# Kernel optimization log

Hardware: AMD Instinct MI355X
Metric: run time of the kernel (lower is better)

The kernel has to match this reference:

```python
import jax, jax.numpy as jnp
import numpy as np

HEADS = 8
DHEAD = 64
KSIZE = 7


def setup_inputs() -> dict:
    key = jax.random.key(0)
    k1, k2, k3, k4 = jax.random.split(key, 4)
    b, H, W, C = 16, 56, 56, 256
    inner = HEADS * DHEAD  # 512
    x = jax.random.normal(k1, (b, H, W, C), jnp.float32)
    Wq = jax.random.normal(k2, (1, 1, C, inner), jnp.float32) * 0.02
    Wkv = jax.random.normal(k3, (KSIZE, KSIZE, C, 2 * inner), jnp.float32) * 0.02
    Wo = jax.random.normal(k4, (1, 1, inner, C), jnp.float32) * 0.02
    bo = jnp.zeros((C,), jnp.float32)
    return {"x": x, "Wq": Wq, "Wkv": Wkv, "Wo": Wo, "bo": bo}


def reference(x, Wq, Wkv, Wo, bo):
    heads, dh = HEADS, DHEAD
    scale = dh ** -0.5
    b, H, W, C = x.shape
    # 1x1 conv Q projection == per-pixel matmul
    q = jnp.einsum('bhwc,cf->bhwf', x, Wq[0, 0])  # [b,H,W,inner]
    # k x k strided conv KV downsample (SAME==VALID since H%k==0)
    kv = jax.lax.conv_general_dilated(
        x, Wkv, window_strides=(KSIZE, KSIZE), padding='VALID',
        dimension_numbers=('NHWC', 'HWIO', 'NHWC'))  # [b,H/k,W/k,2*inner]
    k_, v_ = jnp.split(kv, 2, axis=-1)

    def split_heads(t):
        B, hh, ww, _ = t.shape
        return t.reshape(B, hh * ww, heads, dh)  # [b, seq, h, d]

    q = split_heads(q)      # [b, H*W, h, d]
    k_ = split_heads(k_)    # [b, (H/k)*(W/k), h, d]
    v_ = split_heads(v_)
    dots = jnp.einsum('bqhd,bkhd->bhqk', q, k_) * scale
    attn = jax.nn.softmax(dots, axis=-1)
    out = jnp.einsum('bhqk,bkhd->bqhd', attn, v_)
    out = out.reshape(b, H, W, heads * dh)
    # output 1x1 conv with bias (dropout rate 0 -> identity)
    out = jnp.einsum('bhwf,fc->bhwc', out, Wo[0, 0]) + bo
    return out
```

## Files before the change

### kernel.cpp

```cpp
#include <hip/hip_runtime.h>
#include <stdint.h>

typedef unsigned short ushort_t;
typedef __attribute__((ext_vector_type(8))) unsigned short ushort8v;
typedef __attribute__((ext_vector_type(8))) short short8v;
typedef __attribute__((ext_vector_type(4))) float f32x4;

__device__ __forceinline__ float bf2f(ushort_t u) {
  union { unsigned int i; float f; } v;
  v.i = ((unsigned int)u) << 16;
  return v.f;
}
__device__ __forceinline__ ushort_t f2bf(float f) {
  union { float f; unsigned int i; } v;
  v.f = f;
  unsigned int r = v.i + 0x7FFFu + ((v.i >> 16) & 1u);
  return (ushort_t)(r >> 16);
}

__device__ __forceinline__ ushort8v load8bf(const ushort_t* __restrict__ p) {
  return *(const ushort8v*)p;
}
__device__ __forceinline__ ushort8v load8bf(const float* __restrict__ p) {
  const float4 a = *(const float4*)p;
  const float4 b = *(const float4*)(p + 4);
  ushort8v r;
  r[0] = f2bf(a.x); r[1] = f2bf(a.y); r[2] = f2bf(a.z); r[3] = f2bf(a.w);
  r[4] = f2bf(b.x); r[5] = f2bf(b.y); r[6] = f2bf(b.z); r[7] = f2bf(b.w);
  return r;
}
__device__ __forceinline__ void storeC(float* p, float v) { *p = v; }
__device__ __forceinline__ void storeC(ushort_t* p, float v) { *p = f2bf(v); }

__device__ __forceinline__ void gl16(const ushort_t* g, ushort_t* l) {
  __builtin_amdgcn_global_load_lds(
      (const __attribute__((address_space(1))) void*)g,
      (__attribute__((address_space(3))) void*)l, 16, 0, 0);
}

__device__ __forceinline__ size_t pp_off(unsigned g) {
  const unsigned b = g / 3136u;
  const unsigned r = g - b * 3136u;
  const unsigned y = r / 56u, xx = r - y * 56u;
  const unsigned ty = y / 7u, dy = y - ty * 7u;
  const unsigned tx = xx / 7u, dx = xx - tx * 7u;
  return ((size_t)((b * 64u + ty * 8u + tx) * 49u + dy * 7u + dx)) << 8;
}

__global__ __launch_bounds__(256) void transpose_cvt(
    const float* __restrict__ W, ushort_t* __restrict__ WT, int K, int N) {
  __shared__ float tile[32][33];
  const int t = threadIdx.x;
  const int k0 = blockIdx.y * 32;
  const int n0 = blockIdx.x * 32;
  {
    const int r = t >> 3, c4 = (t & 7) * 4;
    const float4 v = *(const float4*)(W + (size_t)(k0 + r) * N + n0 + c4);
    tile[r][c4] = v.x; tile[r][c4 + 1] = v.y;
    tile[r][c4 + 2] = v.z; tile[r][c4 + 3] = v.w;
  }
  __syncthreads();
  {
    const int rn = t >> 3, ck = (t & 7) * 4;
    union { ushort_t u[4]; uint2 v; } o;
#pragma unroll
    for (int j = 0; j < 4; ++j) o.u[j] = f2bf(tile[ck + j][rn]);
    *(uint2*)(WT + (size_t)(n0 + rn) * K + k0 + ck) = o.v;
  }
}

__global__ __launch_bounds__(256) void cvt_f32_bf16(
    const float* __restrict__ in, ushort_t* __restrict__ out) {
  const int i = (blockIdx.x * 256 + threadIdx.x) * 4;
  const float4 v = *(const float4*)(in + i);
  union { ushort_t u[4]; uint2 q; } o;
  o.u[0] = f2bf(v.x); o.u[1] = f2bf(v.y);
  o.u[2] = f2bf(v.z); o.u[3] = f2bf(v.w);
  *(uint2*)(out + i) = o.q;
}

__global__ __launch_bounds__(256) void cvt_im2col(
    const float* __restrict__ x, ushort_t* __restrict__ xp) {
  const int e = (blockIdx.x * 256 + threadIdx.x) * 8;
  const unsigned p = ((unsigned)e) >> 8;
  const int c = e & 255;
  const float4 a = *(const float4*)(x + e);
  const float4 b = *(const float4*)(x + e + 4);
  ushort8v o;
  o[0] = f2bf(a.x); o[1] = f2bf(a.y); o[2] = f2bf(a.z); o[3] = f2bf(a.w);
  o[4] = f2bf(b.x); o[5] = f2bf(b.y); o[6] = f2bf(b.z); o[7] = f2bf(b.w);
  *(ushort8v*)(xp + pp_off(p) + c) = o;
}

template <int MODE, bool PERMA>
__device__ __forceinline__ void gemm_body(
    const ushort_t* __restrict__ A, const ushort_t* __restrict__ BT,
    const float* __restrict__ bias, void* __restrict__ Cv,
    int N, int K, int m0, int n0, int kbeg, int kend) {
  __shared__ ushort_t lA[2][4096];
  __shared__ ushort_t lB[2][4096];
  const int t = threadIdx.x;
  const int lane = t & 63;
  const int wv = __builtin_amdgcn_readfirstlane(t >> 6);
  const int wm = wv >> 1, wn = wv & 1;
  const int rl = lane & 15;
  const int kof = (lane >> 4) * 8;

  const ushort_t* aS[2];
  const ushort_t* bS[2];
#pragma unroll
  for (int h = 0; h < 2; ++h) {
    const int row = h * 64 + wv * 16 + rl;
    size_t aoff;
    if (PERMA)
      aoff = pp_off((unsigned)(m0 + row));
    else
      aoff = (size_t)(m0 + row) * K;
    aS[h] = A + aoff + kof;
    bS[h] = BT + (size_t)(n0 + row) * K + kof;
  }

  f32x4 acc[4][4] = {};

#pragma unroll
  for (int h = 0; h < 2; ++h) {
    gl16(aS[h] + kbeg, &lA[0][h * 2048 + wv * 512]);
    gl16(bS[h] + kbeg, &lB[0][h * 2048 + wv * 512]);
  }
  __syncthreads();

  int cur = 0;
  for (int k0 = kbeg; k0 < kend; k0 += 32) {
    const int nxt = k0 + 32;
    if (nxt < kend) {
#pragma unroll
      for (int h = 0; h < 2; ++h) {
        gl16(aS[h] + nxt, &lA[cur ^ 1][h * 2048 + wv * 512]);
        gl16(bS[h] + nxt, &lB[cur ^ 1][h * 2048 + wv * 512]);
      }
    }
    short8v af[4], bfr[4];
#pragma unroll
    for (int i = 0; i < 4; ++i) {
      af[i] = *(const short8v*)&lA[cur][(wm * 4 + i) * 512 + lane * 8];
      bfr[i] = *(const short8v*)&lB[cur][(wn * 4 + i) * 512 + lane * 8];
    }
#pragma unroll
    for (int i = 0; i < 4; ++i)
#pragma unroll
      for (int j = 0; j < 4; ++j)
        acc[i][j] = __builtin_amdgcn_mfma_f32_16x16x32_bf16(
            af[i], bfr[j], acc[i][j], 0, 0, 0);
    __syncthreads();
    cur ^= 1;
  }

  const int col = lane & 15, rq = (lane >> 4) * 4;
#pragma unroll
  for (int i = 0; i < 4; ++i) {
    const int mb = m0 + (wm * 4 + i) * 16 + rq;
#pragma unroll
    for (int j = 0; j < 4; ++j) {
      const int nb = n0 + (wn * 4 + j) * 16 + col;
      if (MODE == 0) {
        ushort_t* C = (ushort_t*)Cv;
#pragma unroll
        for (int r = 0; r < 4; ++r)
          C[(size_t)(mb + r) * N + nb] = f2bf(acc[i][j][r]);
      } else if (MODE == 1) {
        float* C = (float*)Cv;
        const float badd = bias[nb];
#pragma unroll
        for (int r = 0; r < 4; ++r)
          C[(size_t)(mb + r) * N + nb] = acc[i][j][r] + badd;
      } else {
        float* C = (float*)Cv;
#pragma unroll
        for (int r = 0; r < 4; ++r)
          atomicAdd(&C[(size_t)(mb + r) * N + nb], acc[i][j][r]);
      }
    }
  }
}

template <int MODE, bool PERMA>
__global__ __launch_bounds__(256) void gemm_nt_2d(
    const ushort_t* __restrict__ A, const ushort_t* __restrict__ BT,
    const float* __restrict__ bias, void* __restrict__ C, int N, int K) {
  gemm_body<MODE, PERMA>(A, BT, bias, C, N, K, blockIdx.y * 128,
                         blockIdx.x * 128, 0, K);
}

__global__ __launch_bounds__(256) void gemm_kv_gl(
    const ushort_t* __restrict__ xpat, const ushort_t* __restrict__ WkvT,
    float* __restrict__ C) {
  const int bl = blockIdx.x;
  const int kbeg = (bl >> 6) * 448;
  gemm_body<2, false>(xpat, WkvT, (const float*)nullptr, C, 1024, 12544,
                      (bl & 7) * 128, ((bl >> 3) & 7) * 128, kbeg, kbeg + 448);
}

template <typename TA, typename TC>
__global__ __launch_bounds__(256) void gemm_mfma_nt(
    const TA* __restrict__ A, const ushort_t* __restrict__ BT,
    const float* __restrict__ bias, TC* __restrict__ C,
    int M, int N, int K, int has_bias) {
  __shared__ ushort_t lA[8 * 512];
  __shared__ ushort_t lB[8 * 512];
  const int t = threadIdx.x;
  const int m0 = blockIdx.y * 128;
  const int n0 = blockIdx.x * 128;
  const int lane = t & 63;
  const int wm = (t >> 6) >> 1, wn = (t >> 6) & 1;

  f32x4 acc[4][4] = {};

  const int sm = t >> 2;
  const int kq = t & 3;

  for (int k0 = 0; k0 < K; k0 += 32) {
#pragma unroll
    for (int h = 0; h < 2; ++h) {
      const int m = h * 64 + sm;
      const int off = (m >> 4) * 512 + (kq * 16 + (m & 15)) * 8;
      const ushort8v av = load8bf(A + (size_t)(m0 + m) * K + k0 + kq * 8);
      *(ushort8v*)&lA[off] = av;
      const ushort8v bv = load8bf(BT + (size_t)(n0 + m) * K + k0 + kq * 8);
      *(ushort8v*)&lB[off] = bv;
    }
    __syncthreads();
    short8v af[4], bf[4];
#pragma unroll
    for (int i = 0; i < 4; ++i) {
      af[i] = *(const short8v*)&lA[(wm * 4 + i) * 512 + lane * 8];
      bf[i] = *(const short8v*)&lB[(wn * 4 + i) * 512 + lane * 8];
    }
#pragma unroll
    for (int i = 0; i < 4; ++i)
#pragma unroll
      for (int j = 0; j < 4; ++j)
        acc[i][j] = __builtin_amdgcn_mfma_f32_16x16x32_bf16(
            af[i], bf[j], acc[i][j], 0, 0, 0);
    __syncthreads();
  }

  const int col = lane & 15, rq = (lane >> 4) * 4;
#pragma unroll
  for (int i = 0; i < 4; ++i) {
    const int mb = m0 + (wm * 4 + i) * 16 + rq;
#pragma unroll
    for (int j = 0; j < 4; ++j) {
      const int nb = n0 + (wn * 4 + j) * 16 + col;
      const float badd = has_bias ? bias[nb] : 0.f;
#pragma unroll
      for (int r = 0; r < 4; ++r)
        storeC(&C[(size_t)(mb + r) * N + nb], acc[i][j][r] + badd);
    }
  }
}

template <typename TA>
__global__ __launch_bounds__(256) void gemm_kv_mfma(
    const TA* __restrict__ x, const ushort_t* __restrict__ WkvT,
    float* __restrict__ C) {
  __shared__ ushort_t lA[8 * 512];
  __shared__ ushort_t lB[8 * 512];
  const int t = threadIdx.x;
  const int bl = blockIdx.x;
  const int m0 = (bl & 7) * 128;
  const int n0 = ((bl >> 3) & 7) * 128;
  const int kbeg = (bl >> 6) * 896;
  const int lane = t & 63;
  const int wm = (t >> 6) >> 1, wn = (t >> 6) & 1;

  f32x4 acc[4][4] = {};

  const int sm = t >> 2;
  const int kq = t & 3;

  for (int k0 = kbeg; k0 < kbeg + 896; k0 += 32) {
#pragma unroll
    for (int h = 0; h < 2; ++h) {
      const int m = h * 64 + sm;
      const int off = (m >> 4) * 512 + (kq * 16 + (m & 15)) * 8;
      const int gm = m0 + m;
      const int b = gm >> 6, ty = (gm >> 3) & 7, tx = gm & 7;
      const int k = k0 + kq * 8;
      const int patch = k >> 8;
      const int c = k & 255;
      const int dy = (patch * 37) >> 8;
      const int dx = patch - dy * 7;
      const int pix = b * 3136 + (ty * 7 + dy) * 56 + (tx * 7 + dx);
      const ushort8v av = load8bf(x + (size_t)pix * 256 + c);
      *(ushort8v*)&lA[off] = av;
      const ushort8v bv =
          load8bf(WkvT + (size_t)(n0 + m) * 12544 + k0 + kq * 8);
      *(ushort8v*)&lB[off] = bv;
    }
    __syncthreads();
    short8v af[4], bf[4];
#pragma unroll
    for (int i = 0; i < 4; ++i) {
      af[i] = *(const short8v*)&lA[(wm * 4 + i) * 512 + lane * 8];
      bf[i] = *(const short8v*)&lB[(wn * 4 + i) * 512 + lane * 8];
    }
#pragma unroll
    for (int i = 0; i < 4; ++i)
#pragma unroll
      for (int j = 0; j < 4; ++j)
        acc[i][j] = __builtin_amdgcn_mfma_f32_16x16x32_bf16(
            af[i], bf[j], acc[i][j], 0, 0, 0);
    __syncthreads();
  }

  const int col = lane & 15, rq = (lane >> 4) * 4;
#pragma unroll
  for (int i = 0; i < 4; ++i) {
    const int mb = m0 + (wm * 4 + i) * 16 + rq;
#pragma unroll
    for (int j = 0; j < 4; ++j) {
      const int nb = n0 + (wn * 4 + j) * 16 + col;
#pragma unroll
      for (int r = 0; r < 4; ++r)
        atomicAdd(&C[(size_t)(mb + r) * 1024 + nb], acc[i][j][r]);
    }
  }
}

__global__ __launch_bounds__(256) void attn_mfma(
    ushort_t* __restrict__ qo, const ushort_t* __restrict__ kvb) {
  __shared__ ushort_t VT[64][72];
  __shared__ ushort_t P[4][64][72];
  const int t = threadIdx.x;
  const int lane = t & 63;
  const int w = t >> 6;
  const int bh = blockIdx.y;
  const int b = bh >> 3, h = bh & 7;
  const ushort_t* kvp = kvb + (size_t)(b * 64) * 1024 + h * 64;

  for (int i = t; i < 512; i += 256) {
    const int key = i >> 3, d0 = (i & 7) * 8;
    const ushort8v v = *(const ushort8v*)(kvp + (size_t)key * 1024 + 512 + d0);
#pragma unroll
    for (int jj = 0; jj < 8; ++jj) VT[d0 + jj][key] = v[jj];
  }
  __syncthreads();

  const int q0_raw = blockIdx.x * 256 + w * 64;
  const bool valid = q0_raw < 3136;
  const int q0 = valid ? q0_raw : 3072;
  const size_t qbase = ((size_t)b * 3136 + q0) * 512 + h * 64;

  const int lm = lane & 15, quad = lane >> 4;

  short8v qf[4][2], kf[4][2];
#pragma unroll
  for (int i = 0; i < 4; ++i)
#pragma unroll
    for (int s = 0; s < 2; ++s) {
      qf[i][s] = *(const short8v*)(qo + qbase + (size_t)(16 * i + lm) * 512 +
                                   32 * s + quad * 8);
      kf[i][s] = *(const short8v*)(kvp + (size_t)(16 * i + lm) * 1024 +
                                   32 * s + quad * 8);
    }

  f32x4 sa[4][4];
#pragma unroll
  for (int i = 0; i < 4; ++i)
#pragma unroll
    for (int j = 0; j < 4; ++j) {
      f32x4 z = {};
      z = __builtin_amdgcn_mfma_f32_16x16x32_bf16(qf[i][0], kf[j][0], z, 0, 0, 0);
      sa[i][j] = __builtin_amdgcn_mfma_f32_16x16x32_bf16(qf[i][1], kf[j][1], z, 0, 0, 0);
    }

  float l[4][4];
#pragma unroll
  for (int i = 0; i < 4; ++i)
#pragma unroll
    for (int r = 0; r < 4; ++r) {
      float m = fmaxf(fmaxf(sa[i][0][r], sa[i][1][r]),
                      fmaxf(sa[i][2][r], sa[i][3][r]));
#pragma unroll
      for (int off = 1; off < 16; off <<= 1) m = fmaxf(m, __shfl_xor(m, off));
      float sum = 0.f;
#pragma unroll
      for (int j = 0; j < 4; ++j) {
        const float p = __expf(0.125f * (sa[i][j][r] - m));
        sa[i][j][r] = p;
        sum += p;
      }
#pragma unroll
      for (int off = 1; off < 16; off <<= 1) sum += __shfl_xor(sum, off);
      l[i][r] = sum;
    }

#pragma unroll
  for (int i = 0; i < 4; ++i) {
    const int row = 16 * i + quad * 4;
#pragma unroll
    for (int j = 0; j < 4; ++j) {
      const int col = 16 * j + lm;
#pragma unroll
      for (int r = 0; r < 4; ++r) P[w][row + r][col] = f2bf(sa[i][j][r]);
    }
  }
  __syncthreads();

  short8v vf[4][2];
#pragma unroll
  for (int jn = 0; jn < 4; ++jn)
#pragma unroll
    for (int s2 = 0; s2 < 2; ++s2)
      vf[jn][s2] = *(const short8v*)&VT[16 * jn + lm][32 * s2 + quad * 8];

  f32x4 oa[4][4];
#pragma unroll
  for (int i = 0; i < 4; ++i) {
    const short8v pf0 = *(const short8v*)&P[w][16 * i + lm][quad * 8];
    const short8v pf1 = *(const short8v*)&P[w][16 * i + lm][32 + quad * 8];
#pragma unroll
    for (int jn = 0; jn < 4; ++jn) {
      f32x4 z = {};
      z = __builtin_amdgcn_mfma_f32_16x16x32_bf16(pf0, vf[jn][0], z, 0, 0, 0);
      oa[i][jn] = __builtin_amdgcn_mfma_f32_16x16x32_bf16(pf1, vf[jn][1], z, 0, 0, 0);
    }
  }

  if (valid) {
#pragma unroll
    for (int i = 0; i < 4; ++i) {
#pragma unroll
      for (int r = 0; r < 4; ++r) {
        const float inv = 1.f / l[i][r];
        const size_t rowoff = qbase + (size_t)(16 * i + quad * 4 + r) * 512;
#pragma unroll
        for (int jn = 0; jn < 4; ++jn)
          qo[rowoff + 16 * jn + lm] = f2bf(oa[i][jn][r] * inv);
      }
    }
  }
}

extern "C" void kernel_launch(void* const* d_in, const int* in_sizes, int n_in,
                              void* d_out, int out_size, void* d_ws,
                              size_t ws_size, hipStream_t stream) {
  const float* x = (const float*)d_in[0];
  const float* Wq = (const float*)d_in[1];
  const float* Wkv = (const float*)d_in[2];
  const float* Wo = (const float*)d_in[3];
  const float* bo = (const float*)d_in[4];
  float* out = (float*)d_out;

  char* ws = (char*)d_ws;
  ushort_t* qbuf = (ushort_t*)(ws);
  float* kvbuf = (float*)(ws + 51380224);
  ushort_t* WkvT = (ushort_t*)(ws + 55574528);
  ushort_t* WqT = (ushort_t*)(ws + 81264640);
  ushort_t* WoT = (ushort_t*)(ws + 81526784);
  ushort_t* kvbf = (ushort_t*)(ws + 81788928);
  ushort_t* xpat = (ushort_t*)(ws + 83886080);
  const bool use_fast = ws_size >= 109576192u;

  hipLaunchKernelGGL(transpose_cvt, dim3(16, 8), dim3(256), 0, stream, Wq, WqT,
                     256, 512);
  hipLaunchKernelGGL(transpose_cvt, dim3(32, 392), dim3(256), 0, stream, Wkv,
                     WkvT, 12544, 1024);
  hipLaunchKernelGGL(transpose_cvt, dim3(8, 16), dim3(256), 0, stream, Wo, WoT,
                     512, 256);
  hipMemsetAsync(kvbuf, 0, 1024 * 1024 * 4, stream);

  if (use_fast) {
    hipLaunchKernelGGL(cvt_im2col, dim3(6272), dim3(256), 0, stream, x, xpat);
    hipLaunchKernelGGL((gemm_nt_2d<0, true>), dim3(4, 392), dim3(256), 0,
                       stream, xpat, WqT, (const float*)nullptr, qbuf, 512,
                       256);
    hipLaunchKernelGGL(gemm_kv_gl, dim3(1792), dim3(256), 0, stream, xpat,
                       WkvT, kvbuf);
    hipLaunchKernelGGL(cvt_f32_bf16, dim3(1024), dim3(256), 0, stream, kvbuf,
                       kvbf);
    hipLaunchKernelGGL(attn_mfma, dim3(13, 128), dim3(256), 0, stream, qbuf,
                       kvbf);
    hipLaunchKernelGGL((gemm_nt_2d<1, false>), dim3(2, 392), dim3(256), 0,
                       stream, qbuf, WoT, bo, out, 256, 512);
  } else {
    hipLaunchKernelGGL((gemm_mfma_nt<float, ushort_t>), dim3(4, 392),
                       dim3(256), 0, stream, x, WqT, (const float*)nullptr,
                       qbuf, 50176, 512, 256, 0);
    hipLaunchKernelGGL((gemm_kv_mfma<float>), dim3(896), dim3(256), 0, stream,
                       x, WkvT, kvbuf);
    hipLaunchKernelGGL(cvt_f32_bf16, dim3(1024), dim3(256), 0, stream, kvbuf,
                       kvbf);
    hipLaunchKernelGGL(attn_mfma, dim3(13, 128), dim3(256), 0, stream, qbuf,
                       kvbf);
    hipLaunchKernelGGL((gemm_mfma_nt<ushort_t, float>), dim3(2, 392),
                       dim3(256), 0, stream, qbuf, WoT, bo, out, 50176, 256,
                       512, 1);
  }
}
```

Before: 401.4 us.

## Triple-buffer GEMM LDS pipeline with single barrier and halve KV split-K

The shared GEMM body moves from double to triple LDS buffering. Each iteration now keeps two global-to-LDS loads in flight, using explicit vmcnt waits and a single barrier instead of two __syncthreads per k-step. Separately, the KV split-K GEMM now covers 896-wide K chunks per block with half as many blocks, which halves the atomicAdd traffic into the fp32 accumulator. The costs are more LDS per block, which can lower occupancy, and less parallelism in the KV GEMM.

Measured after the change: 386.0 us. -3.8%, faster.

```diff
diff --git a/kernel.cpp b/kernel.cpp
--- a/kernel.cpp
+++ b/kernel.cpp
@@ -97,8 +97,8 @@
     const ushort_t* __restrict__ A, const ushort_t* __restrict__ BT,
     const float* __restrict__ bias, void* __restrict__ Cv,
     int N, int K, int m0, int n0, int kbeg, int kend) {
-  __shared__ ushort_t lA[2][4096];
-  __shared__ ushort_t lB[2][4096];
+  __shared__ ushort_t lA[3][4096];
+  __shared__ ushort_t lB[3][4096];
   const int t = threadIdx.x;
   const int lane = t & 63;
   const int wv = __builtin_amdgcn_readfirstlane(t >> 6);
@@ -122,28 +122,42 @@
 
   f32x4 acc[4][4] = {};
 
+  const int nst = (kend - kbeg) >> 5;
+
 #pragma unroll
   for (int h = 0; h < 2; ++h) {
     gl16(aS[h] + kbeg, &lA[0][h * 2048 + wv * 512]);
     gl16(bS[h] + kbeg, &lB[0][h * 2048 + wv * 512]);
   }
-  __syncthreads();
-
-  int cur = 0;
-  for (int k0 = kbeg; k0 < kend; k0 += 32) {
-    const int nxt = k0 + 32;
-    if (nxt < kend) {
+#pragma unroll
+  for (int h = 0; h < 2; ++h) {
+    gl16(aS[h] + kbeg + 32, &lA[1][h * 2048 + wv * 512]);
+    gl16(bS[h] + kbeg + 32, &lB[1][h * 2048 + wv * 512]);
+  }
+
+  int bcur = 0;
+  for (int st = 0; st < nst; ++st) {
+    if (st + 1 < nst)
+      asm volatile("s_waitcnt vmcnt(4)" ::: "memory");
+    else
+      asm volatile("s_waitcnt vmcnt(0)" ::: "memory");
+    __builtin_amdgcn_s_barrier();
+
+    if (st + 2 < nst) {
+      const int bpre = (bcur == 0) ? 2 : bcur - 1;
+      const int nk = kbeg + st * 32 + 64;
 #pragma unroll
       for (int h = 0; h < 2; ++h) {
-        gl16(aS[h] + nxt, &lA[cur ^ 1][h * 2048 + wv * 512]);
-        gl16(bS[h] + nxt, &lB[cur ^ 1][h * 2048 + wv * 512]);
+        gl16(aS[h] + nk, &lA[bpre][h * 2048 + wv * 512]);
+        gl16(bS[h] + nk, &lB[bpre][h * 2048 + wv * 512]);
       }
     }
+
     short8v af[4], bfr[4];
 #pragma unroll
     for (int i = 0; i < 4; ++i) {
-      af[i] = *(const short8v*)&lA[cur][(wm * 4 + i) * 512 + lane * 8];
-      bfr[i] = *(const short8v*)&lB[cur][(wn * 4 + i) * 512 + lane * 8];
+      af[i] = *(const short8v*)&lA[bcur][(wm * 4 + i) * 512 + lane * 8];
+      bfr[i] = *(const short8v*)&lB[bcur][(wn * 4 + i) * 512 + lane * 8];
     }
 #pragma unroll
     for (int i = 0; i < 4; ++i)
@@ -151,8 +165,8 @@
       for (int j = 0; j < 4; ++j)
         acc[i][j] = __builtin_amdgcn_mfma_f32_16x16x32_bf16(
             af[i], bfr[j], acc[i][j], 0, 0, 0);
-    __syncthreads();
-    cur ^= 1;
+
+    bcur = (bcur == 2) ? 0 : bcur + 1;
   }
 
   const int col = lane & 15, rq = (lane >> 4) * 4;
@@ -195,9 +209,9 @@
     const ushort_t* __restrict__ xpat, const ushort_t* __restrict__ WkvT,
     float* __restrict__ C) {
   const int bl = blockIdx.x;
-  const int kbeg = (bl >> 6) * 448;
+  const int kbeg = (bl >> 6) * 896;
   gemm_body<2, false>(xpat, WkvT, (const float*)nullptr, C, 1024, 12544,
-                      (bl & 7) * 128, ((bl >> 3) & 7) * 128, kbeg, kbeg + 448);
+                      (bl & 7) * 128, ((bl >> 3) & 7) * 128, kbeg, kbeg + 896);
 }
 
 template <typename TA, typename TC>
@@ -475,7 +489,7 @@
     hipLaunchKernelGGL((gemm_nt_2d<0, true>), dim3(4, 392), dim3(256), 0,
                        stream, xpat, WqT, (const float*)nullptr, qbuf, 512,
                        256);
-    hipLaunchKernelGGL(gemm_kv_gl, dim3(1792), dim3(256), 0, stream, xpat,
+    hipLaunchKernelGGL(gemm_kv_gl, dim3(896), dim3(256), 0, stream, xpat,
                        WkvT, kvbuf);
     hipLaunchKernelGGL(cvt_f32_bf16, dim3(1024), dim3(256), 0, stream, kvbuf,
                        kvbf);
```

## Replace direct global-to-LDS loads with register-staged prefetch and halve KV split-K

Applied to the files above, without the earlier changes.

The GEMM body stops using global_load_lds DMA into LDS. It now loads the next K-slice into registers, runs the MFMAs on the current slice, and then writes the prefetched data to the alternate LDS buffer with a new per-thread layout. Separately, the KV split-K chunk is doubled from 448 to 896, which halves the KV GEMM grid and the number of atomic accumulation passes. The change trades LDS DMA for register pressure and extra VGPR-to-LDS stores, and the KV GEMM now has fewer blocks to fill the device.

Result: faster. 342.7 us (-14.6%).

```diff
diff --git a/kernel.cpp b/kernel.cpp
--- a/kernel.cpp
+++ b/kernel.cpp
@@ -31,12 +31,6 @@
 }
 __device__ __forceinline__ void storeC(float* p, float v) { *p = v; }
 __device__ __forceinline__ void storeC(ushort_t* p, float v) { *p = f2bf(v); }
-
-__device__ __forceinline__ void gl16(const ushort_t* g, ushort_t* l) {
-  __builtin_amdgcn_global_load_lds(
-      (const __attribute__((address_space(1))) void*)g,
-      (__attribute__((address_space(3))) void*)l, 16, 0, 0);
-}
 
 __device__ __forceinline__ size_t pp_off(unsigned g) {
   const unsigned b = g / 3136u;
@@ -101,44 +95,53 @@
   __shared__ ushort_t lB[2][4096];
   const int t = threadIdx.x;
   const int lane = t & 63;
-  const int wv = __builtin_amdgcn_readfirstlane(t >> 6);
-  const int wm = wv >> 1, wn = wv & 1;
-  const int rl = lane & 15;
-  const int kof = (lane >> 4) * 8;
-
-  const ushort_t* aS[2];
-  const ushort_t* bS[2];
+  const int wm = (t >> 6) >> 1, wn = (t >> 6) & 1;
+  const int sm = t >> 2;
+  const int kq = t & 3;
+
+  const ushort_t* aR[2];
+  const ushort_t* bR[2];
+  int off[2];
 #pragma unroll
   for (int h = 0; h < 2; ++h) {
-    const int row = h * 64 + wv * 16 + rl;
+    const int m = h * 64 + sm;
+    off[h] = (m >> 4) * 512 + (kq * 16 + (m & 15)) * 8;
     size_t aoff;
     if (PERMA)
-      aoff = pp_off((unsigned)(m0 + row));
+      aoff = pp_off((unsigned)(m0 + m));
     else
-      aoff = (size_t)(m0 + row) * K;
-    aS[h] = A + aoff + kof;
-    bS[h] = BT + (size_t)(n0 + row) * K + kof;
+      aoff = (size_t)(m0 + m) * K;
+    aR[h] = A + aoff + kq * 8;
+    bR[h] = BT + (size_t)(n0 + m) * K + kq * 8;
   }
 
   f32x4 acc[4][4] = {};
-
+  const int nst = (kend - kbeg) >> 5;
+
+  ushort8v av[2], bv[2];
 #pragma unroll
   for (int h = 0; h < 2; ++h) {
-    gl16(aS[h] + kbeg, &lA[0][h * 2048 + wv * 512]);
-    gl16(bS[h] + kbeg, &lB[0][h * 2048 + wv * 512]);
+    av[h] = *(const ushort8v*)(aR[h] + kbeg);
+    bv[h] = *(const ushort8v*)(bR[h] + kbeg);
+  }
+#pragma unroll
+  for (int h = 0; h < 2; ++h) {
+    *(ushort8v*)&lA[0][off[h]] = av[h];
+    *(ushort8v*)&lB[0][off[h]] = bv[h];
   }
   __syncthreads();
 
-  int cur = 0;
-  for (int k0 = kbeg; k0 < kend; k0 += 32) {
-    const int nxt = k0 + 32;
-    if (nxt < kend) {
+  for (int st = 0; st < nst; ++st) {
+    const int cur = st & 1;
+    if (st + 1 < nst) {
+      const int nk = kbeg + (st + 1) * 32;
 #pragma unroll
       for (int h = 0; h < 2; ++h) {
-        gl16(aS[h] + nxt, &lA[cur ^ 1][h * 2048 + wv * 512]);
-        gl16(bS[h] + nxt, &lB[cur ^ 1][h * 2048 + wv * 512]);
+        av[h] = *(const ushort8v*)(aR[h] + nk);
+        bv[h] = *(const ushort8v*)(bR[h] + nk);
       }
     }
+
     short8v af[4], bfr[4];
 #pragma unroll
     for (int i = 0; i < 4; ++i) {
@@ -151,8 +154,15 @@
       for (int j = 0; j < 4; ++j)
         acc[i][j] = __builtin_amdgcn_mfma_f32_16x16x32_bf16(
             af[i], bfr[j], acc[i][j], 0, 0, 0);
+
+    if (st + 1 < nst) {
+#pragma unroll
+      for (int h = 0; h < 2; ++h) {
+        *(ushort8v*)&lA[cur ^ 1][off[h]] = av[h];
+        *(ushort8v*)&lB[cur ^ 1][off[h]] = bv[h];
+      }
+    }
     __syncthreads();
-    cur ^= 1;
   }
 
   const int col = lane & 15, rq = (lane >> 4) * 4;
@@ -195,9 +205,9 @@
     const ushort_t* __restrict__ xpat, const ushort_t* __restrict__ WkvT,
     float* __restrict__ C) {
   const int bl = blockIdx.x;
-  const int kbeg = (bl >> 6) * 448;
+  const int kbeg = (bl >> 6) * 896;
   gemm_body<2, false>(xpat, WkvT, (const float*)nullptr, C, 1024, 12544,
-                      (bl & 7) * 128, ((bl >> 3) & 7) * 128, kbeg, kbeg + 448);
+                      (bl & 7) * 128, ((bl >> 3) & 7) * 128, kbeg, kbeg + 896);
 }
 
 template <typename TA, typename TC>
@@ -475,7 +485,7 @@
     hipLaunchKernelGGL((gemm_nt_2d<0, true>), dim3(4, 392), dim3(256), 0,
                        stream, xpat, WqT, (const float*)nullptr, qbuf, 512,
                        256);
-    hipLaunchKernelGGL(gemm_kv_gl, dim3(1792), dim3(256), 0, stream, xpat,
+    hipLaunchKernelGGL(gemm_kv_gl, dim3(896), dim3(256), 0, stream, xpat,
                        WkvT, kvbuf);
     hipLaunchKernelGGL(cvt_f32_bf16, dim3(1024), dim3(256), 0, stream, kvbuf,
                        kvbf);
```
